# Optimization experiments

Measured on AMD Instinct MI355X. Metric: run time of the kernel, lower is better.

Reference implementation:

```python
import jax, jax.numpy as jnp
import numpy as np

N = 50000      # nodes
E = 1600000    # edges
F_IN = 128     # input_dim
H = 160        # hidden_dim
G = 512        # graphs in batch
C = 2          # num_classes
EPS = 1e-5     # BatchNorm eps


def setup_inputs() -> dict:
    key = jax.random.key(0)
    ks = jax.random.split(key, 12)
    x = jax.random.normal(ks[0], (N, F_IN), jnp.float32)
    edge_index = jax.random.randint(ks[1], (2, E), 0, N, dtype=jnp.int32)
    batch = jnp.sort(jax.random.randint(ks[2], (N,), 0, G, dtype=jnp.int32))

    def lin(k, fi, fo):
        s = 1.0 / np.sqrt(fi)
        kw, kb = jax.random.split(k)
        W = jax.random.uniform(kw, (fi, fo), jnp.float32, -s, s)
        b = jax.random.uniform(kb, (fo,), jnp.float32, -s, s)
        return W, b

    W1, b1 = lin(ks[3], F_IN, H)
    W2, b2 = lin(ks[4], H, H)
    W3, b3 = lin(ks[5], H, H)
    Wc1, bc1 = lin(ks[6], H, H // 2)
    Wc2, bc2 = lin(ks[7], H // 2, C)

    def bn(k):
        k1, k2, k3, k4 = jax.random.split(k, 4)
        gamma = jax.random.uniform(k1, (H,), jnp.float32, 0.5, 1.5)
        beta = jax.random.normal(k2, (H,), jnp.float32) * 0.1
        mean = jax.random.normal(k3, (H,), jnp.float32) * 0.1
        var = jax.random.uniform(k4, (H,), jnp.float32, 0.5, 1.5)
        return gamma, beta, mean, var

    g1, be1, m1, v1 = bn(ks[8])
    g2, be2, m2, v2 = bn(ks[9])
    g3, be3, m3, v3 = bn(ks[10])

    return dict(x=x, edge_index=edge_index, batch=batch,
                W1=W1, b1=b1, W2=W2, b2=b2, W3=W3, b3=b3,
                g1=g1, be1=be1, m1=m1, v1=v1,
                g2=g2, be2=be2, m2=m2, v2=v2,
                g3=g3, be3=be3, m3=m3, v3=v3,
                Wc1=Wc1, bc1=bc1, Wc2=Wc2, bc2=bc2)


def gcn_conv(x, W, b, src, dst):
    """PyG GCNConv: symmetric deg normalization with self-loops; lin -> aggregate -> +bias."""
    n = x.shape[0]
    h = x @ W                                   # [N, H]
    loop = jnp.arange(n, dtype=src.dtype)
    s = jnp.concatenate([src, loop])            # self-loops appended
    d = jnp.concatenate([dst, loop])
    deg = jax.ops.segment_sum(jnp.ones_like(d, jnp.float32), d, num_segments=n)
    inv = jnp.where(deg > 0, jax.lax.rsqrt(deg), 0.0)
    msg = h[s] * (inv[s] * inv[d])[:, None]     # [E+N, H] gather + norm
    return jax.ops.segment_sum(msg, d, num_segments=n) + b


def bn_eval(x, gamma, beta, mean, var):
    return (x - mean) * jax.lax.rsqrt(var + EPS) * gamma + beta


def reference(x, edge_index, batch, W1, b1, W2, b2, W3, b3,
              g1, be1, m1, v1, g2, be2, m2, v2, g3, be3, m3, v3,
              Wc1, bc1, Wc2, bc2):
    src, dst = edge_index[0], edge_index[1]
    # eval mode: dropout is identity, BN uses running stats
    h = jax.nn.relu(bn_eval(gcn_conv(x, W1, b1, src, dst), g1, be1, m1, v1))
    h = jax.nn.relu(bn_eval(gcn_conv(h, W2, b2, src, dst), g2, be2, m2, v2))
    h = jax.nn.relu(bn_eval(gcn_conv(h, W3, b3, src, dst), g3, be3, m3, v3))
    # global mean pool over graph ids
    sums = jax.ops.segment_sum(h, batch, num_segments=G)
    cnt = jax.ops.segment_sum(jnp.ones((h.shape[0],), jnp.float32), batch, num_segments=G)
    pooled = sums / jnp.clip(cnt, 1.0)[:, None]
    # MLP head
    z = jax.nn.relu(pooled @ Wc1 + bc1)
    return z @ Wc2 + bc2
```

## Files before the change

kernel.cpp:

```cpp
#include <hip/hip_runtime.h>

#define N_NODES   50000
#define N_EDGES   1600000
#define FDIM_IN   128
#define HDIM      160
#define N_GRAPHS  512
#define BN_EPS    1e-5f
#define NBKT_MAX  128

typedef short  frag8 __attribute__((ext_vector_type(8)));
typedef float  facc4 __attribute__((ext_vector_type(4)));


__device__ __forceinline__ unsigned short f2bf(float f) {
    unsigned int u = __float_as_uint(f);
    return (unsigned short)((u + 0x7FFFu + ((u >> 16) & 1u)) >> 16);
}

__device__ __forceinline__ unsigned int pack2(float lo, float hi) {
    return (unsigned int)f2bf(lo) | ((unsigned int)f2bf(hi) << 16);
}

__device__ __forceinline__ void addpk(float* acc, uint4 r) {
    acc[0] += __uint_as_float(r.x << 16);
    acc[1] += __uint_as_float(r.x & 0xFFFF0000u);
    acc[2] += __uint_as_float(r.y << 16);
    acc[3] += __uint_as_float(r.y & 0xFFFF0000u);
    acc[4] += __uint_as_float(r.z << 16);
    acc[5] += __uint_as_float(r.z & 0xFFFF0000u);
    acc[6] += __uint_as_float(r.w << 16);
    acc[7] += __uint_as_float(r.w & 0xFFFF0000u);
}


__global__ __launch_bounds__(256) void coarse_hist_kernel(const int* __restrict__ dst,
                                                          int* __restrict__ cg, int E) {
    __shared__ int h[NBKT_MAX];
    int tid = threadIdx.x;
    if (tid < NBKT_MAX) h[tid] = 0;
    __syncthreads();
    for (int e = blockIdx.x * 256 + tid; e < E; e += gridDim.x * 256)
        atomicAdd(&h[dst[e] >> 9], 1);
    __syncthreads();
    if (tid < NBKT_MAX && h[tid]) atomicAdd(&cg[tid], h[tid]);
}

__global__ __launch_bounds__(128) void coarse_scan_kernel(const int* __restrict__ cg,
                                                          int* __restrict__ bucket_base,
                                                          int* __restrict__ bucket_cursor) {
    __shared__ int h[NBKT_MAX];
    int t = threadIdx.x;
    h[t] = cg[t];
    __syncthreads();
    if (t == 0) {
        int run = 0;
        for (int i = 0; i < NBKT_MAX; ++i) { int c = h[i]; h[i] = run; run += c; }
    }
    __syncthreads();
    bucket_base[t] = h[t];
    bucket_cursor[t] = h[t];
    if (t == 0) bucket_base[NBKT_MAX] = h[NBKT_MAX - 1] + cg[NBKT_MAX - 1];
}

__global__ __launch_bounds__(256) void part_kernel(const int* __restrict__ src,
                                                   const int* __restrict__ dst,
                                                   int* __restrict__ bucket_cursor,
                                                   unsigned int* __restrict__ pairs, int E) {
    __shared__ int bcnt[NBKT_MAX], bbase[NBKT_MAX], lc[NBKT_MAX];
    int tid = threadIdx.x;
    int per = (E + gridDim.x - 1) / gridDim.x;
    int beg = blockIdx.x * per;
    int end = min(beg + per, E);
    if (tid < NBKT_MAX) { bcnt[tid] = 0; lc[tid] = 0; }
    __syncthreads();
    for (int e = beg + tid; e < end; e += 256)
        atomicAdd(&bcnt[dst[e] >> 9], 1);
    __syncthreads();
    if (tid < NBKT_MAX)
        bbase[tid] = bcnt[tid] ? atomicAdd(&bucket_cursor[tid], bcnt[tid]) : 0;
    __syncthreads();
    for (int e = beg + tid; e < end; e += 256) {
        int d = dst[e];
        int b = d >> 9;
        int pos = bbase[b] + atomicAdd(&lc[b], 1);
        pairs[pos] = ((unsigned int)src[e] << 9) | (unsigned int)(d & 511);
    }
}

__global__ __launch_bounds__(1024) void bucket_csr_kernel(const unsigned int* __restrict__ pairs,
                                                          const int* __restrict__ bucket_base,
                                                          int* __restrict__ row_off,
                                                          float* __restrict__ inv,
                                                          int* __restrict__ ssrc, int n) {
    __shared__ int h[512];
    __shared__ int ws[8];
    int tid = threadIdx.x;
    int b = blockIdx.x;
    int node0 = b << 9;
    int beg = bucket_base[b], end = bucket_base[b + 1];
    if (tid < 512) h[tid] = 0;
    __syncthreads();
    for (int j = beg + tid; j < end; j += 1024)
        atomicAdd(&h[pairs[j] & 511], 1);
    __syncthreads();
    int cntv = (tid < 512) ? h[tid] : 0;
    __syncthreads();
    int lane = tid & 63, wid = tid >> 6;
    int incl = cntv;
    #pragma unroll
    for (int off = 1; off < 64; off <<= 1) {
        int u = __shfl_up(incl, off);
        if (lane >= off) incl += u;
    }
    if (tid < 512 && lane == 63) ws[wid] = incl;
    __syncthreads();
    if (tid == 0) {
        int r = 0;
        #pragma unroll
        for (int i = 0; i < 8; ++i) { int t = ws[i]; ws[i] = r; r += t; }
    }
    __syncthreads();
    int excl = (tid < 512) ? (ws[wid] + incl - cntv) : 0;
    if (tid < 512) {
        int node = node0 + tid;
        if (node < n) {
            row_off[node] = beg + excl;
            inv[node] = rsqrtf((float)(cntv + 1));
        }
        h[tid] = excl;
    }
    if (tid == 0 && (node0 + 512) >= n) row_off[n] = end;
    __syncthreads();
    for (int j = beg + tid; j < end; j += 1024) {
        unsigned int p = pairs[j];
        int pos = beg + atomicAdd(&h[p & 511], 1);
        ssrc[pos] = (int)(p >> 9);
    }
}


struct PrepArgs {
    const float *b, *g, *be, *m, *v;
    float *sc, *sh;
};

__global__ void prep3_kernel(PrepArgs a0, PrepArgs a1, PrepArgs a2) {
    PrepArgs a = (blockIdx.x == 0) ? a0 : (blockIdx.x == 1) ? a1 : a2;
    int t = threadIdx.x;
    if (t < HDIM) {
        float s = a.g[t] * rsqrtf(a.v[t] + BN_EPS);
        a.sc[t] = s;
        a.sh[t] = (a.b[t] - a.m[t]) * s + a.be[t];
    }
}


__global__ __launch_bounds__(256) void pack_w3_kernel(const float* __restrict__ W1,
                                                      const float* __restrict__ W2,
                                                      const float* __restrict__ W3,
                                                      unsigned short* __restrict__ o1,
                                                      unsigned short* __restrict__ o2,
                                                      unsigned short* __restrict__ o3) {
    int tid = blockIdx.x * 256 + threadIdx.x;
    const float* W;
    unsigned short* o;
    int i;
    if (tid < 128 * 160)             { W = W1; o = o1; i = tid; }
    else if (tid < 128 * 160 + 160 * 160) { W = W2; o = o2; i = tid - 128 * 160; }
    else if (tid < 128 * 160 + 2 * 160 * 160) { W = W3; o = o3; i = tid - (128 * 160 + 160 * 160); }
    else return;
    int j = i & 7;
    int l = (i >> 3) & 63;
    int u = (i >> 9) % 10;
    int t = i / 5120;
    int k = t * 32 + (l >> 4) * 8 + j;
    int nn = u * 16 + (l & 15);
    o[i] = f2bf(W[k * 160 + nn]);
}


__global__ __launch_bounds__(256) void scale_bf16_kernel(const float* __restrict__ x,
                                                         const float* __restrict__ inv,
                                                         unsigned short* __restrict__ out,
                                                         int n) {
    int i = blockIdx.x * 256 + threadIdx.x;
    if (i < n * 32) {
        int node = i >> 5;
        float w = inv[node];
        float4 v = ((const float4*)x)[i];
        ushort4 o;
        o.x = f2bf(v.x * w); o.y = f2bf(v.y * w);
        o.z = f2bf(v.z * w); o.w = f2bf(v.w * w);
        ((ushort4*)out)[i] = o;
    }
}


template <int C>
__global__ __launch_bounds__(256) void agg_grp_kernel(const unsigned short* __restrict__ in_s,
                                                      const float* __restrict__ inv,
                                                      const int* __restrict__ row_off,
                                                      const int* __restrict__ ssrc,
                                                      unsigned short* __restrict__ out, int n) {
    constexpr int LPR = C / 8;
    constexpr int G   = 64 / LPR;
    constexpr int RB  = C * 2;
    int wave = threadIdx.x >> 6;
    int lane = threadIdx.x & 63;
    int node = blockIdx.x * 4 + wave;
    if (node >= n) return;
    int g  = lane / LPR;
    int cl = lane - g * LPR;
    bool act = g < G;
    int beg = row_off[node], end = row_off[node + 1];
    const char* base = (const char*)in_s;
    int lb = cl * 16;

    float acc[8];
    #pragma unroll
    for (int i = 0; i < 8; ++i) acc[i] = 0.f;

    if (g == 0) {
        uint4 r = *(const uint4*)(base + (size_t)node * RB + lb);
        addpk(acc, r);
    }

    int e = act ? beg + g : end;

    for (; e + 7 * G < end; e += 8 * G) {
        int s0 = ssrc[e],         s1 = ssrc[e + G];
        int s2 = ssrc[e + 2 * G], s3 = ssrc[e + 3 * G];
        int s4 = ssrc[e + 4 * G], s5 = ssrc[e + 5 * G];
        int s6 = ssrc[e + 6 * G], s7 = ssrc[e + 7 * G];
        uint4 r0 = *(const uint4*)(base + (size_t)s0 * RB + lb);
        uint4 r1 = *(const uint4*)(base + (size_t)s1 * RB + lb);
        uint4 r2 = *(const uint4*)(base + (size_t)s2 * RB + lb);
        uint4 r3 = *(const uint4*)(base + (size_t)s3 * RB + lb);
        uint4 r4 = *(const uint4*)(base + (size_t)s4 * RB + lb);
        uint4 r5 = *(const uint4*)(base + (size_t)s5 * RB + lb);
        uint4 r6 = *(const uint4*)(base + (size_t)s6 * RB + lb);
        uint4 r7 = *(const uint4*)(base + (size_t)s7 * RB + lb);
        addpk(acc, r0); addpk(acc, r1); addpk(acc, r2); addpk(acc, r3);
        addpk(acc, r4); addpk(acc, r5); addpk(acc, r6); addpk(acc, r7);
    }
    if (e + 3 * G < end) {
        int s0 = ssrc[e],         s1 = ssrc[e + G];
        int s2 = ssrc[e + 2 * G], s3 = ssrc[e + 3 * G];
        uint4 r0 = *(const uint4*)(base + (size_t)s0 * RB + lb);
        uint4 r1 = *(const uint4*)(base + (size_t)s1 * RB + lb);
        uint4 r2 = *(const uint4*)(base + (size_t)s2 * RB + lb);
        uint4 r3 = *(const uint4*)(base + (size_t)s3 * RB + lb);
        addpk(acc, r0); addpk(acc, r1); addpk(acc, r2); addpk(acc, r3);
        e += 4 * G;
    }
    if (e + G < end) {
        int s0 = ssrc[e], s1 = ssrc[e + G];
        uint4 r0 = *(const uint4*)(base + (size_t)s0 * RB + lb);
        uint4 r1 = *(const uint4*)(base + (size_t)s1 * RB + lb);
        addpk(acc, r0); addpk(acc, r1);
        e += 2 * G;
    }
    if (e < end) {
        uint4 r = *(const uint4*)(base + (size_t)ssrc[e] * RB + lb);
        addpk(acc, r);
    }

    if (G == 4) {
        #pragma unroll
        for (int i = 0; i < 8; ++i) acc[i] += __shfl(acc[i], lane + 32);
        #pragma unroll
        for (int i = 0; i < 8; ++i) acc[i] += __shfl(acc[i], lane + 16);
    } else {
        #pragma unroll
        for (int i = 0; i < 8; ++i) {
            float a = __shfl(acc[i], lane + 20);
            float b = __shfl(acc[i], lane + 40);
            acc[i] += a + b;
        }
    }

    if (lane < LPR) {
        float wi = inv[node];
        uint4 o;
        o.x = pack2(acc[0] * wi, acc[1] * wi);
        o.y = pack2(acc[2] * wi, acc[3] * wi);
        o.z = pack2(acc[4] * wi, acc[5] * wi);
        o.w = pack2(acc[6] * wi, acc[7] * wi);
        *(uint4*)((char*)out + (size_t)node * RB + lb) = o;
    }
}


template <int K, int OUTMODE>
__global__ __launch_bounds__(256) void mfma_gemm_kernel(const unsigned short* __restrict__ A,
                                                        const unsigned short* __restrict__ Bp,
                                                        const float* __restrict__ sc,
                                                        const float* __restrict__ sh,
                                                        const float* __restrict__ inv,
                                                        float* __restrict__ CoutF,
                                                        unsigned short* __restrict__ CoutB,
                                                        int n) {
    constexpr int KT = K / 32;
    int tid = threadIdx.x;
    int wave = tid >> 6, lane = tid & 63;
    int row0 = blockIdx.x * 64 + wave * 16;
    int m = lane & 15, q = lane >> 4;

    int arow = row0 + m;
    int arowc = (arow < n) ? arow : (n - 1);
    const frag8* Abase = (const frag8*)(A + (size_t)arowc * K);
    const frag8* Bbase = (const frag8*)Bp;

    facc4 acc[10];
    #pragma unroll
    for (int u = 0; u < 10; ++u) acc[u] = (facc4){0.f, 0.f, 0.f, 0.f};

    #pragma unroll
    for (int t = 0; t < KT; ++t) {
        frag8 af = Abase[t * 4 + q];
        #pragma unroll
        for (int u = 0; u < 10; ++u) {
            frag8 bf = Bbase[(t * 10 + u) * 64 + lane];
            acc[u] = __builtin_amdgcn_mfma_f32_16x16x32_bf16(af, bf, acc[u], 0, 0, 0);
        }
    }

    #pragma unroll
    for (int u = 0; u < 10; ++u) {
        int c = u * 16 + m;
        float scv = sc[c], shv = sh[c];
        #pragma unroll
        for (int r = 0; r < 4; ++r) {
            int rr = row0 + q * 4 + r;
            if (rr < n) {
                float v = fmaxf(acc[u][r] * scv + shv, 0.f);
                if (OUTMODE == 1) {
                    CoutB[(size_t)rr * 160 + c] = f2bf(v * inv[rr]);
                } else {
                    CoutF[(size_t)rr * 160 + c] = v;
                }
            }
        }
    }
}


__global__ __launch_bounds__(256) void pool_head_kernel(const float* __restrict__ h,
                                                        const int* __restrict__ batch,
                                                        const float* __restrict__ Wc1,
                                                        const float* __restrict__ bc1,
                                                        const float* __restrict__ Wc2,
                                                        const float* __restrict__ bc2,
                                                        float* __restrict__ out, int n) {
    __shared__ float pooled[160];
    __shared__ float z[80];
    __shared__ int range[2];
    int g = blockIdx.x;
    int t = threadIdx.x;
    if (t < 2) {
        int target = g + t;
        int lo = 0, hi = n;
        while (lo < hi) {
            int mid = (lo + hi) >> 1;
            if (batch[mid] < target) lo = mid + 1; else hi = mid;
        }
        range[t] = lo;
    }
    __syncthreads();
    int lo = range[0], hi = range[1];
    if (t < 160) {
        float s = 0.f;
        for (int r = lo; r < hi; ++r) s += h[(size_t)r * 160 + t];
        pooled[t] = s / fmaxf((float)(hi - lo), 1.f);
    }
    __syncthreads();
    if (t < 80) {
        float s = bc1[t];
        for (int k = 0; k < 160; ++k) s += pooled[k] * Wc1[k * 80 + t];
        z[t] = fmaxf(s, 0.f);
    }
    __syncthreads();
    if (t < 2) {
        float s = bc2[t];
        for (int k = 0; k < 80; ++k) s += z[k] * Wc2[k * 2 + t];
        out[g * 2 + t] = s;
    }
}


static inline size_t align256(size_t x) { return (x + 255) & ~(size_t)255; }

extern "C" void kernel_launch(void* const* d_in, const int* in_sizes, int n_in,
                              void* d_out, int out_size, void* d_ws, size_t ws_size,
                              hipStream_t stream) {
    const float* x   = (const float*)d_in[0];
    const int* ei    = (const int*)d_in[1];
    const int* batch = (const int*)d_in[2];
    const float* W1  = (const float*)d_in[3];
    const float* b1  = (const float*)d_in[4];
    const float* W2  = (const float*)d_in[5];
    const float* b2  = (const float*)d_in[6];
    const float* W3  = (const float*)d_in[7];
    const float* b3  = (const float*)d_in[8];
    const float* g1  = (const float*)d_in[9];
    const float* be1 = (const float*)d_in[10];
    const float* m1  = (const float*)d_in[11];
    const float* v1  = (const float*)d_in[12];
    const float* g2  = (const float*)d_in[13];
    const float* be2 = (const float*)d_in[14];
    const float* m2  = (const float*)d_in[15];
    const float* v2  = (const float*)d_in[16];
    const float* g3  = (const float*)d_in[17];
    const float* be3 = (const float*)d_in[18];
    const float* m3  = (const float*)d_in[19];
    const float* v3  = (const float*)d_in[20];
    const float* Wc1 = (const float*)d_in[21];
    const float* bc1 = (const float*)d_in[22];
    const float* Wc2 = (const float*)d_in[23];
    const float* bc2 = (const float*)d_in[24];
    float* out = (float*)d_out;

    const int N = in_sizes[2];
    const int E = in_sizes[1] / 2;
    const int* src = ei;
    const int* dst = ei + E;

    char* w = (char*)d_ws;
    int*   row_off = (int*)w;             w += align256((size_t)(N + 1) * 4);
    float* inv     = (float*)w;           w += align256((size_t)N * 4);
    int*   ssrc    = (int*)w;             w += align256((size_t)E * 4);
    unsigned int* pairs = (unsigned int*)w; w += align256((size_t)E * 4);
    int*   cg      = (int*)w;             w += align256((size_t)NBKT_MAX * 4);
    int*   bucket_base   = (int*)w;       w += align256((size_t)(NBKT_MAX + 1) * 4);
    int*   bucket_cursor = (int*)w;       w += align256((size_t)NBKT_MAX * 4);
    float* scsh    = (float*)w;           w += align256((size_t)6 * HDIM * 4);
    unsigned short* W1p = (unsigned short*)w;  w += align256((size_t)FDIM_IN * HDIM * 2);
    unsigned short* W2p = (unsigned short*)w;  w += align256((size_t)HDIM * HDIM * 2);
    unsigned short* W3p = (unsigned short*)w;  w += align256((size_t)HDIM * HDIM * 2);
    unsigned short* bufA_bf = (unsigned short*)w;  w += align256((size_t)N * HDIM * 2);
    char* regionR = w;
    unsigned short* xs_bf = (unsigned short*)regionR;
    unsigned short* hs_bf = (unsigned short*)(regionR + align256((size_t)N * FDIM_IN * 2));
    float* bufB = (float*)regionR;
    float* sc1 = scsh, *sh1 = scsh + 160, *sc2 = scsh + 320, *sh2 = scsh + 480,
         * sc3 = scsh + 640, *sh3 = scsh + 800;

    hipMemsetAsync(cg, 0, (size_t)NBKT_MAX * 4, stream);

    coarse_hist_kernel<<<256, 256, 0, stream>>>(dst, cg, E);
    coarse_scan_kernel<<<1, 128, 0, stream>>>(cg, bucket_base, bucket_cursor);
    part_kernel<<<256, 256, 0, stream>>>(src, dst, bucket_cursor, pairs, E);
    int nbkt = (N + 511) >> 9;
    bucket_csr_kernel<<<nbkt, 1024, 0, stream>>>(pairs, bucket_base, row_off, inv, ssrc, N);

    PrepArgs pa0 = {b1, g1, be1, m1, v1, sc1, sh1};
    PrepArgs pa1 = {b2, g2, be2, m2, v2, sc2, sh2};
    PrepArgs pa2 = {b3, g3, be3, m3, v3, sc3, sh3};
    prep3_kernel<<<3, 256, 0, stream>>>(pa0, pa1, pa2);
    pack_w3_kernel<<<(128 * 160 + 2 * 160 * 160 + 255) / 256, 256, 0, stream>>>(W1, W2, W3, W1p, W2p, W3p);

    int gAgg = (N + 3) / 4;
    int gGemm = (N + 63) / 64;

    scale_bf16_kernel<<<(N * 32 + 255) / 256, 256, 0, stream>>>(x, inv, xs_bf, N);
    agg_grp_kernel<128><<<gAgg, 256, 0, stream>>>(xs_bf, inv, row_off, ssrc, bufA_bf, N);
    mfma_gemm_kernel<128, 1><<<gGemm, 256, 0, stream>>>(bufA_bf, W1p, sc1, sh1, inv, nullptr, hs_bf, N);
    agg_grp_kernel<160><<<gAgg, 256, 0, stream>>>(hs_bf, inv, row_off, ssrc, bufA_bf, N);
    mfma_gemm_kernel<160, 1><<<gGemm, 256, 0, stream>>>(bufA_bf, W2p, sc2, sh2, inv, nullptr, hs_bf, N);
    agg_grp_kernel<160><<<gAgg, 256, 0, stream>>>(hs_bf, inv, row_off, ssrc, bufA_bf, N);
    mfma_gemm_kernel<160, 0><<<gGemm, 256, 0, stream>>>(bufA_bf, W3p, sc3, sh3, inv, bufB, nullptr, N);

    pool_head_kernel<<<N_GRAPHS, 256, 0, stream>>>(bufB, batch, Wc1, bc1, Wc2, bc2, out, N);
}
```

Measured before the change: 470.0 us.

## Store bf16 features in 32-column slices and aggregate one slice per block

Node features move from a row-major layout to 32-column slices (64 bytes per node per slice). The scale, GEMM-output and GEMM-input code is rewritten to read and write this layout. Aggregation now launches one block group per slice, with 4 lanes per row and 4 edge groups per node, so each slice's gather working set (about 3.2 MB) fits in cache. The cost is that the edge index list is read 4-5 times instead of once, and the edge loop unrolls less deeply, so fewer loads are in flight. Nontemporal loads and stores are added for the edge indices and the aggregate output.

```diff
diff --git a/kernel.cpp b/kernel.cpp
--- a/kernel.cpp
+++ b/kernel.cpp
@@ -10,6 +10,7 @@
 
 typedef short  frag8 __attribute__((ext_vector_type(8)));
 typedef float  facc4 __attribute__((ext_vector_type(4)));
+typedef unsigned int u32x4 __attribute__((ext_vector_type(4)));
 
 
 __device__ __forceinline__ unsigned short f2bf(float f) {
@@ -186,107 +187,79 @@
     int i = blockIdx.x * 256 + threadIdx.x;
     if (i < n * 32) {
         int node = i >> 5;
+        int q4 = i & 31;
         float w = inv[node];
         float4 v = ((const float4*)x)[i];
         ushort4 o;
         o.x = f2bf(v.x * w); o.y = f2bf(v.y * w);
         o.z = f2bf(v.z * w); o.w = f2bf(v.w * w);
-        ((ushort4*)out)[i] = o;
-    }
-}
-
-
-template <int C>
-__global__ __launch_bounds__(256) void agg_grp_kernel(const unsigned short* __restrict__ in_s,
-                                                      const float* __restrict__ inv,
-                                                      const int* __restrict__ row_off,
-                                                      const int* __restrict__ ssrc,
-                                                      unsigned short* __restrict__ out, int n) {
-    constexpr int LPR = C / 8;
-    constexpr int G   = 64 / LPR;
-    constexpr int RB  = C * 2;
+        int sl = q4 >> 3;
+        int cc = (q4 & 7) * 4;
+        size_t sstr = (size_t)n * 32;
+        *(ushort4*)(out + (size_t)sl * sstr + (size_t)node * 32 + cc) = o;
+    }
+}
+
+
+__global__ __launch_bounds__(256) void agg_slice_kernel(const unsigned short* __restrict__ in_s,
+                                                        const float* __restrict__ inv,
+                                                        const int* __restrict__ row_off,
+                                                        const int* __restrict__ ssrc,
+                                                        unsigned short* __restrict__ out,
+                                                        int n, int bpS) {
+    int s  = blockIdx.x / bpS;
+    int nb = blockIdx.x - s * bpS;
     int wave = threadIdx.x >> 6;
     int lane = threadIdx.x & 63;
-    int node = blockIdx.x * 4 + wave;
+    int j  = lane >> 4;
+    int gg = (lane >> 2) & 3;
+    int cl = lane & 3;
+    int node = nb * 16 + wave * 4 + j;
     if (node >= n) return;
-    int g  = lane / LPR;
-    int cl = lane - g * LPR;
-    bool act = g < G;
+
+    size_t sstr = (size_t)n * 32;
+    const char* base = (const char*)(in_s + (size_t)s * sstr);
     int beg = row_off[node], end = row_off[node + 1];
-    const char* base = (const char*)in_s;
     int lb = cl * 16;
 
     float acc[8];
     #pragma unroll
     for (int i = 0; i < 8; ++i) acc[i] = 0.f;
 
-    if (g == 0) {
-        uint4 r = *(const uint4*)(base + (size_t)node * RB + lb);
+    if (gg == 0) {
+        uint4 r = *(const uint4*)(base + (size_t)node * 64 + lb);
         addpk(acc, r);
     }
 
-    int e = act ? beg + g : end;
-
-    for (; e + 7 * G < end; e += 8 * G) {
-        int s0 = ssrc[e],         s1 = ssrc[e + G];
-        int s2 = ssrc[e + 2 * G], s3 = ssrc[e + 3 * G];
-        int s4 = ssrc[e + 4 * G], s5 = ssrc[e + 5 * G];
-        int s6 = ssrc[e + 6 * G], s7 = ssrc[e + 7 * G];
-        uint4 r0 = *(const uint4*)(base + (size_t)s0 * RB + lb);
-        uint4 r1 = *(const uint4*)(base + (size_t)s1 * RB + lb);
-        uint4 r2 = *(const uint4*)(base + (size_t)s2 * RB + lb);
-        uint4 r3 = *(const uint4*)(base + (size_t)s3 * RB + lb);
-        uint4 r4 = *(const uint4*)(base + (size_t)s4 * RB + lb);
-        uint4 r5 = *(const uint4*)(base + (size_t)s5 * RB + lb);
-        uint4 r6 = *(const uint4*)(base + (size_t)s6 * RB + lb);
-        uint4 r7 = *(const uint4*)(base + (size_t)s7 * RB + lb);
-        addpk(acc, r0); addpk(acc, r1); addpk(acc, r2); addpk(acc, r3);
-        addpk(acc, r4); addpk(acc, r5); addpk(acc, r6); addpk(acc, r7);
-    }
-    if (e + 3 * G < end) {
-        int s0 = ssrc[e],         s1 = ssrc[e + G];
-        int s2 = ssrc[e + 2 * G], s3 = ssrc[e + 3 * G];
-        uint4 r0 = *(const uint4*)(base + (size_t)s0 * RB + lb);
-        uint4 r1 = *(const uint4*)(base + (size_t)s1 * RB + lb);
-        uint4 r2 = *(const uint4*)(base + (size_t)s2 * RB + lb);
-        uint4 r3 = *(const uint4*)(base + (size_t)s3 * RB + lb);
-        addpk(acc, r0); addpk(acc, r1); addpk(acc, r2); addpk(acc, r3);
-        e += 4 * G;
-    }
-    if (e + G < end) {
-        int s0 = ssrc[e], s1 = ssrc[e + G];
-        uint4 r0 = *(const uint4*)(base + (size_t)s0 * RB + lb);
-        uint4 r1 = *(const uint4*)(base + (size_t)s1 * RB + lb);
-        addpk(acc, r0); addpk(acc, r1);
-        e += 2 * G;
+    int e = beg + gg;
+    for (; e + 4 < end; e += 8) {
+        int s0 = __builtin_nontemporal_load(&ssrc[e]);
+        int s1 = __builtin_nontemporal_load(&ssrc[e + 4]);
+        uint4 r0 = *(const uint4*)(base + (size_t)s0 * 64 + lb);
+        uint4 r1 = *(const uint4*)(base + (size_t)s1 * 64 + lb);
+        addpk(acc, r0);
+        addpk(acc, r1);
     }
     if (e < end) {
-        uint4 r = *(const uint4*)(base + (size_t)ssrc[e] * RB + lb);
+        int s0 = __builtin_nontemporal_load(&ssrc[e]);
+        uint4 r = *(const uint4*)(base + (size_t)s0 * 64 + lb);
         addpk(acc, r);
     }
 
-    if (G == 4) {
-        #pragma unroll
-        for (int i = 0; i < 8; ++i) acc[i] += __shfl(acc[i], lane + 32);
-        #pragma unroll
-        for (int i = 0; i < 8; ++i) acc[i] += __shfl(acc[i], lane + 16);
-    } else {
-        #pragma unroll
-        for (int i = 0; i < 8; ++i) {
-            float a = __shfl(acc[i], lane + 20);
-            float b = __shfl(acc[i], lane + 40);
-            acc[i] += a + b;
-        }
-    }
-
-    if (lane < LPR) {
+    #pragma unroll
+    for (int i = 0; i < 8; ++i) {
+        acc[i] += __shfl_xor(acc[i], 4);
+        acc[i] += __shfl_xor(acc[i], 8);
+    }
+
+    if (gg == 0) {
         float wi = inv[node];
-        uint4 o;
+        u32x4 o;
         o.x = pack2(acc[0] * wi, acc[1] * wi);
         o.y = pack2(acc[2] * wi, acc[3] * wi);
         o.z = pack2(acc[4] * wi, acc[5] * wi);
         o.w = pack2(acc[6] * wi, acc[7] * wi);
-        *(uint4*)((char*)out + (size_t)node * RB + lb) = o;
+        __builtin_nontemporal_store(o, (u32x4*)((char*)(out + (size_t)s * sstr) + (size_t)node * 64 + lb));
     }
 }
 
@@ -308,7 +281,7 @@
 
     int arow = row0 + m;
     int arowc = (arow < n) ? arow : (n - 1);
-    const frag8* Abase = (const frag8*)(A + (size_t)arowc * K);
+    size_t sstr = (size_t)n * 32;
     const frag8* Bbase = (const frag8*)Bp;
 
     facc4 acc[10];
@@ -317,7 +290,7 @@
 
     #pragma unroll
     for (int t = 0; t < KT; ++t) {
-        frag8 af = Abase[t * 4 + q];
+        frag8 af = *(const frag8*)(A + (size_t)t * sstr + (size_t)arowc * 32 + q * 8);
         #pragma unroll
         for (int u = 0; u < 10; ++u) {
             frag8 bf = Bbase[(t * 10 + u) * 64 + lane];
@@ -335,7 +308,7 @@
             if (rr < n) {
                 float v = fmaxf(acc[u][r] * scv + shv, 0.f);
                 if (OUTMODE == 1) {
-                    CoutB[(size_t)rr * 160 + c] = f2bf(v * inv[rr]);
+                    CoutB[(size_t)(c >> 5) * sstr + (size_t)rr * 32 + (c & 31)] = f2bf(v * inv[rr]);
                 } else {
                     CoutF[(size_t)rr * 160 + c] = v;
                 }
@@ -445,7 +418,7 @@
     float* sc1 = scsh, *sh1 = scsh + 160, *sc2 = scsh + 320, *sh2 = scsh + 480,
          * sc3 = scsh + 640, *sh3 = scsh + 800;
 
-    hipMemsetAsync(cg, 0, (size_t)NBKT_MAX * 4, stream);
+    (void)hipMemsetAsync(cg, 0, (size_t)NBKT_MAX * 4, stream);
 
     coarse_hist_kernel<<<256, 256, 0, stream>>>(dst, cg, E);
     coarse_scan_kernel<<<1, 128, 0, stream>>>(cg, bucket_base, bucket_cursor);
@@ -459,15 +432,15 @@
     prep3_kernel<<<3, 256, 0, stream>>>(pa0, pa1, pa2);
     pack_w3_kernel<<<(128 * 160 + 2 * 160 * 160 + 255) / 256, 256, 0, stream>>>(W1, W2, W3, W1p, W2p, W3p);
 
-    int gAgg = (N + 3) / 4;
+    int bpS = (N + 15) / 16;
     int gGemm = (N + 63) / 64;
 
     scale_bf16_kernel<<<(N * 32 + 255) / 256, 256, 0, stream>>>(x, inv, xs_bf, N);
-    agg_grp_kernel<128><<<gAgg, 256, 0, stream>>>(xs_bf, inv, row_off, ssrc, bufA_bf, N);
+    agg_slice_kernel<<<bpS * 4, 256, 0, stream>>>(xs_bf, inv, row_off, ssrc, bufA_bf, N, bpS);
     mfma_gemm_kernel<128, 1><<<gGemm, 256, 0, stream>>>(bufA_bf, W1p, sc1, sh1, inv, nullptr, hs_bf, N);
-    agg_grp_kernel<160><<<gAgg, 256, 0, stream>>>(hs_bf, inv, row_off, ssrc, bufA_bf, N);
+    agg_slice_kernel<<<bpS * 5, 256, 0, stream>>>(hs_bf, inv, row_off, ssrc, bufA_bf, N, bpS);
     mfma_gemm_kernel<160, 1><<<gGemm, 256, 0, stream>>>(bufA_bf, W2p, sc2, sh2, inv, nullptr, hs_bf, N);
-    agg_grp_kernel<160><<<gAgg, 256, 0, stream>>>(hs_bf, inv, row_off, ssrc, bufA_bf, N);
+    agg_slice_kernel<<<bpS * 5, 256, 0, stream>>>(hs_bf, inv, row_off, ssrc, bufA_bf, N, bpS);
     mfma_gemm_kernel<160, 0><<<gGemm, 256, 0, stream>>>(bufA_bf, W3p, sc3, sh3, inv, bufB, nullptr, N);
 
     pool_head_kernel<<<N_GRAPHS, 256, 0, stream>>>(bufB, batch, Wc1, bc1, Wc2, bc2, out, N);
```

Result: slower. 511.3 us (+8.8%).
